# Kernel optimization log

Measured on AMD Instinct MI355X. Metric: run time of the kernel, lower is better.

## Reference

```python
import jax, jax.numpy as jnp
import numpy as np

B, T, C, H = 4, 4096, 1024, 128

def setup_inputs() -> dict:
    key = jax.random.key(0)
    k1, k2, k3, k4 = jax.random.split(key, 4)
    ix = jax.random.normal(k1, (B, T, C), dtype=jnp.float32)
    Wq = jax.random.normal(k2, (C, H), dtype=jnp.float32) * (C ** -0.5)
    Wk = jax.random.normal(k3, (C, H), dtype=jnp.float32) * (C ** -0.5)
    Wv = jax.random.normal(k4, (C, H), dtype=jnp.float32) * (C ** -0.5)
    return {"ix": ix, "Wq": Wq, "Wk": Wk, "Wv": Wv}

def reference(ix, Wq, Wk, Wv):
    Bc, Tc, Cc = ix.shape
    q = ix @ Wq                      # [B,T,H]
    k = ix @ Wk                      # [B,T,H]
    v = ix @ Wv                      # [B,T,H]
    # NOTE: original computes k @ q^T (row index from k, col index from q),
    # scaled by n_embed**-0.5 (C, not head_size).
    wei = jnp.einsum('bth,bsh->bts', k, q) * (Cc ** -0.5)  # [B,T,T]
    causal = jnp.tril(jnp.ones((Tc, Tc), dtype=bool))
    wei = jnp.where(causal[None, :, :], wei, -jnp.inf)
    wei = jax.nn.softmax(wei, axis=-1)
    # dropout is identity in eval mode
    out = jnp.einsum('bts,bsh->bth', wei, v)  # [B,T,H]
    return out
```

## Files before the change

### kernel.cpp

```cpp
#include <hip/hip_runtime.h>
#include <hip/hip_bf16.h>

typedef __bf16 bf16x8 __attribute__((ext_vector_type(8)));
typedef float f32x4 __attribute__((ext_vector_type(4)));
typedef float f32x16 __attribute__((ext_vector_type(16)));
typedef unsigned u32x4 __attribute__((ext_vector_type(4)));
#define MFMA16 __builtin_amdgcn_mfma_f32_16x16x32_bf16
#define MFMA32 __builtin_amdgcn_mfma_f32_32x32x16_bf16

static constexpr int Bsz = 4, T = 4096, C = 1024, H = 128;
static constexpr int BT = Bsz * T;

__device__ __forceinline__ void gl2lds16(const __bf16* g, __bf16* l) {
    __builtin_amdgcn_global_load_lds(
        (const __attribute__((address_space(1))) void*)g,
        (__attribute__((address_space(3))) void*)l, 16, 0, 0);
}

__device__ __forceinline__ unsigned pk2(float a, float b) {
    unsigned short ua = __builtin_bit_cast(unsigned short, (__bf16)a);
    unsigned short ub = __builtin_bit_cast(unsigned short, (__bf16)b);
    return (unsigned)ua | ((unsigned)ub << 16);
}

__global__ __launch_bounds__(256) void k_wprep(
    const float* __restrict__ Wq, const float* __restrict__ Wk,
    const float* __restrict__ Wv, __bf16* __restrict__ WTall)
{
    int idx = blockIdx.x * 256 + threadIdx.x;
    int n = idx >> 10, k = idx & 1023;
    int mat = n >> 7, col = n & 127;
    const float* W = mat == 0 ? Wq : (mat == 1 ? Wk : Wv);
    float s = (mat == 1) ? 0.045084220f : 1.0f;
    WTall[idx] = (__bf16)(W[k * H + col] * s);
}

__global__ __launch_bounds__(512) void k_proj(
    const float* __restrict__ X, const __bf16* __restrict__ WTall,
    __bf16* __restrict__ Qp, __bf16* __restrict__ Kp, __bf16* __restrict__ VT)
{
    union Smem {
        struct { __bf16 a[2][64 * 64]; __bf16 b[2][192 * 64]; } s;
        __bf16 vt_e[128][72];
    };
    __shared__ Smem su;

    const int tid = threadIdx.x;
    const int lane = tid & 63, w = tid >> 6;
    const int c = lane & 15, hi = lane >> 4;
    const int wm = w >> 2, wn = w & 3;
    const int ny = blockIdx.x >> 8;
    const int m0 = (blockIdx.x & 255) * 64;
    const int xorv = (c & 7) << 3;

    const int arow = tid >> 3, ac8 = tid & 7;
    const float* aSrc = X + (size_t)(m0 + arow) * C + ac8 * 8;
    const int aDst = arow * 64 + ((ac8 * 8) ^ ((arow & 7) << 3));
    const int brl = lane >> 3, bch = lane & 7;
    const __bf16* Wbase = WTall + (size_t)ny * 192 * 1024;

    f32x4 acc[2][3];
    #pragma unroll
    for (int i = 0; i < 2; ++i)
        #pragma unroll
        for (int j = 0; j < 3; ++j) acc[i][j] = (f32x4){0.f, 0.f, 0.f, 0.f};

    #pragma unroll
    for (int ib = 0; ib < 3; ++ib) {
        int row = w * 24 + ib * 8 + brl;
        int ch = bch ^ (row & 7);
        gl2lds16(Wbase + (size_t)row * 1024 + ch * 8, &su.s.b[0][(w * 3 + ib) * 512]);
    }
    {
        float4 f0 = *(const float4*)aSrc;
        float4 f1 = *(const float4*)(aSrc + 4);
        bf16x8 av;
        av[0] = (__bf16)f0.x; av[1] = (__bf16)f0.y; av[2] = (__bf16)f0.z; av[3] = (__bf16)f0.w;
        av[4] = (__bf16)f1.x; av[5] = (__bf16)f1.y; av[6] = (__bf16)f1.z; av[7] = (__bf16)f1.w;
        *(bf16x8*)&su.s.a[0][aDst] = av;
    }
    __syncthreads();

    for (int t = 0; t < 16; ++t) {
        int cur = t & 1;
        float4 g0, g1;
        if (t < 15) {
            int k0 = (t + 1) * 64;
            #pragma unroll
            for (int ib = 0; ib < 3; ++ib) {
                int row = w * 24 + ib * 8 + brl;
                int ch = bch ^ (row & 7);
                gl2lds16(Wbase + (size_t)row * 1024 + k0 + ch * 8,
                         &su.s.b[cur ^ 1][(w * 3 + ib) * 512]);
            }
            g0 = *(const float4*)(aSrc + k0);
            g1 = *(const float4*)(aSrc + k0 + 4);
        }
        #pragma unroll
        for (int kk = 0; kk < 2; ++kk) {
            bf16x8 a0 = *(const bf16x8*)&su.s.a[cur][(wm * 32 + c) * 64 + ((kk * 32 + hi * 8) ^ xorv)];
            bf16x8 a1 = *(const bf16x8*)&su.s.a[cur][(wm * 32 + 16 + c) * 64 + ((kk * 32 + hi * 8) ^ xorv)];
            #pragma unroll
            for (int fn = 0; fn < 3; ++fn) {
                bf16x8 bb = *(const bf16x8*)&su.s.b[cur][(wn * 48 + fn * 16 + c) * 64 + ((kk * 32 + hi * 8) ^ xorv)];
                acc[0][fn] = MFMA16(a0, bb, acc[0][fn], 0, 0, 0);
                acc[1][fn] = MFMA16(a1, bb, acc[1][fn], 0, 0, 0);
            }
        }
        if (t < 15) {
            bf16x8 av;
            av[0] = (__bf16)g0.x; av[1] = (__bf16)g0.y; av[2] = (__bf16)g0.z; av[3] = (__bf16)g0.w;
            av[4] = (__bf16)g1.x; av[5] = (__bf16)g1.y; av[6] = (__bf16)g1.z; av[7] = (__bf16)g1.w;
            *(bf16x8*)&su.s.a[cur ^ 1][aDst] = av;
        }
        __syncthreads();
    }

    #pragma unroll
    for (int mi = 0; mi < 2; ++mi) {
        int rowl = wm * 32 + mi * 16 + hi * 4;
        #pragma unroll
        for (int fn = 0; fn < 3; ++fn) {
            int nb = ny * 192 + wn * 48 + fn * 16;
            int mat = nb >> 7, colb = (nb & 127) + c;
            #pragma unroll
            for (int r = 0; r < 4; ++r) {
                __bf16 v = (__bf16)acc[mi][fn][r];
                if (mat == 0)      Qp[(size_t)(m0 + rowl + r) * H + colb] = v;
                else if (mat == 1) Kp[(size_t)(m0 + rowl + r) * H + colb] = v;
                else               su.vt_e[colb][rowl + r] = v;
            }
        }
    }
    __syncthreads();
    if (ny == 1) {
        int d = tid >> 2, tc = (tid & 3) * 16;
        int b = m0 >> 12, tl = m0 & (T - 1);
        __bf16* dst = VT + ((size_t)b * H + d) * T + tl + tc;
        const __bf16* s2 = &su.vt_e[d][tc];
        *(uint4*)dst = *(const uint4*)s2;
        *(uint4*)(dst + 8) = *(const uint4*)(s2 + 8);
    }
}

__global__ __launch_bounds__(256, 1) void k_attn(
    const __bf16* __restrict__ Ka, const __bf16* __restrict__ Qb,
    const __bf16* __restrict__ VT, float* __restrict__ Out,
    float* __restrict__ Po, float* __restrict__ Pl)
{
    __shared__ float oacc[64][132];
    __shared__ float sml[4][64];

    const int tid = threadIdx.x, lane = tid & 63, w = tid >> 6;
    const int t31 = lane & 31, hi5 = lane >> 5;
    const int ws = w >> 1, sp = w & 1;

    const int bi = blockIdx.x;
    const int p = bi & 1, b = (bi >> 1) & 3, u = bi >> 3;

    const __bf16* Kb  = Ka + (size_t)b * T * H;
    const __bf16* Qbb = Qb + (size_t)b * T * H;
    const __bf16* Vb  = VT + (size_t)b * H * T;

    #pragma unroll 1
    for (int half = 0; half < 2; ++half) {
        const int j  = half ? (63 - u) : u;
        const int t0 = j * 64;
        const int nsteps = j + 1;

        bf16x8 kb2[2][8];
        #pragma unroll
        for (int tt = 0; tt < 2; ++tt)
            #pragma unroll
            for (int kc = 0; kc < 8; ++kc)
                kb2[tt][kc] = *(const bf16x8*)(Kb + (size_t)(t0 + tt * 32 + t31) * H + kc * 16 + hi5 * 8);

        f32x16 oc[2][4];
        #pragma unroll
        for (int tt = 0; tt < 2; ++tt)
            #pragma unroll
            for (int dn = 0; dn < 4; ++dn)
                #pragma unroll
                for (int r = 0; r < 16; ++r) oc[tt][dn][r] = 0.f;
        float ol0 = 0.f, ol1 = 0.f;

        for (int i = p + 2 * sp; i < nsteps; i += 4) {
            const int sbase = i * 64 + ws * 32;
            bf16x8 qa[8];
            #pragma unroll
            for (int kc = 0; kc < 8; ++kc)
                qa[kc] = *(const bf16x8*)(Qbb + (size_t)(sbase + t31) * H + kc * 16 + hi5 * 8);
            bf16x8 vb[4][2];
            #pragma unroll
            for (int dn = 0; dn < 4; ++dn)
                #pragma unroll
                for (int ks = 0; ks < 2; ++ks)
                    vb[dn][ks] = *(const bf16x8*)(Vb + (size_t)(dn * 32 + t31) * T + sbase + ks * 16 + hi5 * 8);

            #pragma unroll
            for (int tt = 0; tt < 2; ++tt) {
                const int tg = t0 + tt * 32 + t31;
                f32x16 accA, accB;
                #pragma unroll
                for (int r = 0; r < 16; ++r) { accA[r] = 0.f; accB[r] = 0.f; }
                #pragma unroll
                for (int kc = 0; kc < 4; ++kc) accA = MFMA32(qa[kc], kb2[tt][kc], accA, 0, 0, 0);
                #pragma unroll
                for (int kc = 4; kc < 8; ++kc) accB = MFMA32(qa[kc], kb2[tt][kc], accB, 0, 0, 0);

                const bool dz = (sbase + 31 >= t0 + tt * 32);
                float pv[16];
                #pragma unroll
                for (int r = 0; r < 16; ++r) {
                    float e = __builtin_amdgcn_exp2f(accA[r] + accB[r]);
                    if (dz) {
                        int sg = sbase + (r & 3) + 8 * (r >> 2) + 4 * hi5;
                        if (sg > tg) e = 0.f;
                    }
                    pv[r] = e;
                }
                float rs = ((pv[0] + pv[1]) + (pv[2] + pv[3])) + ((pv[4] + pv[5]) + (pv[6] + pv[7]))
                         + ((pv[8] + pv[9]) + (pv[10] + pv[11])) + ((pv[12] + pv[13]) + (pv[14] + pv[15]));
                if (tt == 0) ol0 += rs; else ol1 += rs;

                unsigned x1 = pk2(pv[0], pv[1]),  x2 = pk2(pv[2], pv[3]);
                unsigned y1 = pk2(pv[4], pv[5]),  y2 = pk2(pv[6], pv[7]);
                unsigned x3 = pk2(pv[8], pv[9]),  x4 = pk2(pv[10], pv[11]);
                unsigned y3 = pk2(pv[12], pv[13]), y4 = pk2(pv[14], pv[15]);
                unsigned sx1 = __shfl_xor((int)x1, 32), sx2 = __shfl_xor((int)x2, 32);
                unsigned sy1 = __shfl_xor((int)y1, 32), sy2 = __shfl_xor((int)y2, 32);
                unsigned sx3 = __shfl_xor((int)x3, 32), sx4 = __shfl_xor((int)x4, 32);
                unsigned sy3 = __shfl_xor((int)y3, 32), sy4 = __shfl_xor((int)y4, 32);
                u32x4 wA, wB;
                wA[0] = hi5 ? sy1 : x1;  wA[1] = hi5 ? sy2 : x2;
                wA[2] = hi5 ? y1 : sx1;  wA[3] = hi5 ? y2 : sx2;
                wB[0] = hi5 ? sy3 : x3;  wB[1] = hi5 ? sy4 : x4;
                wB[2] = hi5 ? y3 : sx3;  wB[3] = hi5 ? y4 : sx4;
                bf16x8 paA = __builtin_bit_cast(bf16x8, wA);
                bf16x8 paB = __builtin_bit_cast(bf16x8, wB);

                #pragma unroll
                for (int dn = 0; dn < 4; ++dn) {
                    oc[tt][dn] = MFMA32(paA, vb[dn][0], oc[tt][dn], 0, 0, 0);
                    oc[tt][dn] = MFMA32(paB, vb[dn][1], oc[tt][dn], 0, 0, 0);
                }
            }
        }

        ol0 += __shfl_xor(ol0, 32);
        ol1 += __shfl_xor(ol1, 32);
        if (lane < 32) { sml[w][t31] = ol0; sml[w][32 + t31] = ol1; }

        for (int g = 0; g < 4; ++g) {
            __syncthreads();
            if (w == g) {
                #pragma unroll
                for (int tt = 0; tt < 2; ++tt)
                    #pragma unroll
                    for (int dn = 0; dn < 4; ++dn)
                        #pragma unroll
                        for (int r = 0; r < 16; ++r) {
                            int row = tt * 32 + (r & 3) + 8 * (r >> 2) + 4 * hi5;
                            int col = dn * 32 + t31;
                            if (g == 0) oacc[row][col]  = oc[tt][dn][r];
                            else        oacc[row][col] += oc[tt][dn][r];
                        }
            }
        }
        __syncthreads();
        {
            int row = tid >> 2, col0 = (tid & 3) * 32;
            float L = sml[0][row] + sml[1][row] + sml[2][row] + sml[3][row];
            float* dst = (p == 0 ? Out : Po) + ((size_t)b * T + t0 + row) * H + col0;
            #pragma unroll
            for (int k = 0; k < 32; k += 4) {
                float4 v;
                v.x = oacc[row][col0 + k];
                v.y = oacc[row][col0 + k + 1];
                v.z = oacc[row][col0 + k + 2];
                v.w = oacc[row][col0 + k + 3];
                *(float4*)(dst + k) = v;
            }
            if ((tid & 3) == 0) Pl[(size_t)p * BT + b * T + t0 + row] = L;
        }
        __syncthreads();
    }
}

__global__ __launch_bounds__(256) void k_merge(
    float* __restrict__ Out, const float* __restrict__ Po,
    const float* __restrict__ Pl)
{
    size_t idx = ((size_t)blockIdx.x * 256 + threadIdx.x) * 8;
    size_t row = idx >> 7;
    float inv = 1.0f / (Pl[row] + Pl[BT + row]);
    float4 a0 = *(const float4*)(Out + idx);
    float4 a1 = *(const float4*)(Out + idx + 4);
    float4 p0 = *(const float4*)(Po + idx);
    float4 p1 = *(const float4*)(Po + idx + 4);
    float4 r0, r1;
    r0.x = (a0.x + p0.x) * inv; r0.y = (a0.y + p0.y) * inv;
    r0.z = (a0.z + p0.z) * inv; r0.w = (a0.w + p0.w) * inv;
    r1.x = (a1.x + p1.x) * inv; r1.y = (a1.y + p1.y) * inv;
    r1.z = (a1.z + p1.z) * inv; r1.w = (a1.w + p1.w) * inv;
    *(float4*)(Out + idx)     = r0;
    *(float4*)(Out + idx + 4) = r1;
}

extern "C" void kernel_launch(void* const* d_in, const int* in_sizes, int n_in,
                              void* d_out, int out_size, void* d_ws, size_t ws_size,
                              hipStream_t stream) {
    const float* ix = (const float*)d_in[0];
    const float* Wq = (const float*)d_in[1];
    const float* Wk = (const float*)d_in[2];
    const float* Wv = (const float*)d_in[3];
    float* out = (float*)d_out;

    __bf16* WTall = (__bf16*)d_ws;
    __bf16* Qp = WTall + 393216;
    __bf16* Kp = Qp + (size_t)BT * H;
    __bf16* VT = Kp + (size_t)BT * H;
    float*  Po = (float*)(VT + (size_t)BT * H);
    float*  Pl = Po + (size_t)BT * H;

    k_wprep<<<dim3(1536), 256, 0, stream>>>(Wq, Wk, Wv, WTall);
    k_proj<<<dim3(512), 512, 0, stream>>>(ix, WTall, Qp, Kp, VT);
    k_attn<<<dim3(256), 256, 0, stream>>>(Kp, Qp, VT, out, Po, Pl);
    k_merge<<<dim3(1024), 256, 0, stream>>>(out, Po, Pl);
}
```

Before: 89.61 us.

## Split attention KV range four ways across 512 blocks with four-way merge

The causal attention kernel now splits each query tile's key/value sweep into four partitions instead of two and launches 512 blocks instead of 256. Launch bounds now allow two blocks per CU, so the MI355X's CUs are better filled. The merge kernel sums four partial outputs and four partial normalizers. In exchange it adds extra fp32 partial-output traffic to workspace and may cost registers under the tighter launch bound, which could cause spills.

New measurement: 125.3 us. +39.9%, slower.

```diff
diff --git a/kernel.cpp b/kernel.cpp
--- a/kernel.cpp
+++ b/kernel.cpp
@@ -143,10 +143,11 @@
     }
 }
 
-__global__ __launch_bounds__(256, 1) void k_attn(
+__global__ __launch_bounds__(256, 2) void k_attn(
     const __bf16* __restrict__ Ka, const __bf16* __restrict__ Qb,
     const __bf16* __restrict__ VT, float* __restrict__ Out,
-    float* __restrict__ Po, float* __restrict__ Pl)
+    float* __restrict__ P1, float* __restrict__ P2, float* __restrict__ P3,
+    float* __restrict__ Pl)
 {
     __shared__ float oacc[64][132];
     __shared__ float sml[4][64];
@@ -156,11 +157,15 @@
     const int ws = w >> 1, sp = w & 1;
 
     const int bi = blockIdx.x;
-    const int p = bi & 1, b = (bi >> 1) & 3, u = bi >> 3;
+    const int plow = bi & 1, b = (bi >> 1) & 3;
+    const int rest = bi >> 3;
+    const int p = ((rest & 1) << 1) | plow;
+    const int u = rest >> 1;
 
     const __bf16* Kb  = Ka + (size_t)b * T * H;
     const __bf16* Qbb = Qb + (size_t)b * T * H;
     const __bf16* Vb  = VT + (size_t)b * H * T;
+    float* dstP = (p == 0) ? Out : (p == 1 ? P1 : (p == 2 ? P2 : P3));
 
     #pragma unroll 1
     for (int half = 0; half < 2; ++half) {
@@ -184,7 +189,7 @@
                 for (int r = 0; r < 16; ++r) oc[tt][dn][r] = 0.f;
         float ol0 = 0.f, ol1 = 0.f;
 
-        for (int i = p + 2 * sp; i < nsteps; i += 4) {
+        for (int i = p + 4 * sp; i < nsteps; i += 8) {
             const int sbase = i * 64 + ws * 32;
             bf16x8 qa[8];
             #pragma unroll
@@ -271,7 +276,7 @@
         {
             int row = tid >> 2, col0 = (tid & 3) * 32;
             float L = sml[0][row] + sml[1][row] + sml[2][row] + sml[3][row];
-            float* dst = (p == 0 ? Out : Po) + ((size_t)b * T + t0 + row) * H + col0;
+            float* dst = dstP + ((size_t)b * T + t0 + row) * H + col0;
             #pragma unroll
             for (int k = 0; k < 32; k += 4) {
                 float4 v;
@@ -288,23 +293,27 @@
 }
 
 __global__ __launch_bounds__(256) void k_merge(
-    float* __restrict__ Out, const float* __restrict__ Po,
+    float* __restrict__ Out, const float* __restrict__ P1,
+    const float* __restrict__ P2, const float* __restrict__ P3,
     const float* __restrict__ Pl)
 {
     size_t idx = ((size_t)blockIdx.x * 256 + threadIdx.x) * 8;
     size_t row = idx >> 7;
-    float inv = 1.0f / (Pl[row] + Pl[BT + row]);
-    float4 a0 = *(const float4*)(Out + idx);
-    float4 a1 = *(const float4*)(Out + idx + 4);
-    float4 p0 = *(const float4*)(Po + idx);
-    float4 p1 = *(const float4*)(Po + idx + 4);
-    float4 r0, r1;
-    r0.x = (a0.x + p0.x) * inv; r0.y = (a0.y + p0.y) * inv;
-    r0.z = (a0.z + p0.z) * inv; r0.w = (a0.w + p0.w) * inv;
-    r1.x = (a1.x + p1.x) * inv; r1.y = (a1.y + p1.y) * inv;
-    r1.z = (a1.z + p1.z) * inv; r1.w = (a1.w + p1.w) * inv;
-    *(float4*)(Out + idx)     = r0;
-    *(float4*)(Out + idx + 4) = r1;
+    float inv = 1.0f / (Pl[row] + Pl[BT + row] + Pl[2 * (size_t)BT + row] + Pl[3 * (size_t)BT + row]);
+    #pragma unroll
+    for (int h = 0; h < 2; ++h) {
+        size_t o = idx + h * 4;
+        float4 a = *(const float4*)(Out + o);
+        float4 q1 = *(const float4*)(P1 + o);
+        float4 q2 = *(const float4*)(P2 + o);
+        float4 q3 = *(const float4*)(P3 + o);
+        float4 r;
+        r.x = (a.x + q1.x + q2.x + q3.x) * inv;
+        r.y = (a.y + q1.y + q2.y + q3.y) * inv;
+        r.z = (a.z + q1.z + q2.z + q3.z) * inv;
+        r.w = (a.w + q1.w + q2.w + q3.w) * inv;
+        *(float4*)(Out + o) = r;
+    }
 }
 
 extern "C" void kernel_launch(void* const* d_in, const int* in_sizes, int n_in,
@@ -320,11 +329,13 @@
     __bf16* Qp = WTall + 393216;
     __bf16* Kp = Qp + (size_t)BT * H;
     __bf16* VT = Kp + (size_t)BT * H;
-    float*  Po = (float*)(VT + (size_t)BT * H);
-    float*  Pl = Po + (size_t)BT * H;
+    float*  P1 = (float*)(VT + (size_t)BT * H);
+    float*  P2 = P1 + (size_t)BT * H;
+    float*  P3 = P2 + (size_t)BT * H;
+    float*  Pl = P3 + (size_t)BT * H;
 
     k_wprep<<<dim3(1536), 256, 0, stream>>>(Wq, Wk, Wv, WTall);
     k_proj<<<dim3(512), 512, 0, stream>>>(ix, WTall, Qp, Kp, VT);
-    k_attn<<<dim3(256), 256, 0, stream>>>(Kp, Qp, VT, out, Po, Pl);
-    k_merge<<<dim3(1024), 256, 0, stream>>>(out, Po, Pl);
-}
+    k_attn<<<dim3(512), 256, 0, stream>>>(Kp, Qp, VT, out, P1, P2, P3, Pl);
+    k_merge<<<dim3(1024), 256, 0, stream>>>(out, P1, P2, P3, Pl);
+}
```
